# Optimization experiments

Hardware: AMD Instinct MI355X
Metric: run time of the kernel (lower is better)

The kernel has to match this reference:

```python
import jax, jax.numpy as jnp
import numpy as np

N, T, P = 4096, 4096, 12  # series, timesteps, seasonality period


def setup_inputs() -> dict:
    key = jax.random.key(0)
    ks = jax.random.split(key, 8)
    return {
        "alpha": jax.random.uniform(ks[0], (N,), dtype=jnp.float32),
        "beta": jax.random.uniform(ks[1], (N,), dtype=jnp.float32),
        "gamma": jax.random.uniform(ks[2], (N,), dtype=jnp.float32),
        "init_level": jax.random.normal(ks[3], (N,), dtype=jnp.float32),
        "init_trend": jax.random.normal(ks[4], (N,), dtype=jnp.float32) * 0.01,
        "init_seasonal": jax.random.normal(ks[5], (N, P), dtype=jnp.float32),
        "obs_noise": jax.random.normal(ks[6], (N, T), dtype=jnp.float32),
        "err": jax.random.normal(ks[7], (N, T), dtype=jnp.float32),
    }


def reference(alpha, beta, gamma, init_level, init_trend, init_seasonal, obs_noise, err):
    """ETS 'AAA' (additive error/trend/seasonal) recurrence, vectorized over N series.

    Per timestep t (matching the torch loop with model_type='AAA'):
      current = level + trend + seasonal[t % P]
      y[t]    = current + obs_noise[t] * 0.1
      level'  = alpha*(current + err[t]) + (1-alpha)*(level + trend)
      trend'  = beta*(level' - level) + (1-beta)*trend
      seasonal[t % P] = gamma*err[t] + (1-gamma)*seasonal[t % P]
    """
    Tlen = obs_noise.shape[1]
    Pn = init_seasonal.shape[1]

    def step(carry, xs):
        level, trend, seasonal = carry  # (N,), (N,), (N, P)
        t, on, e = xs                   # scalar, (N,), (N,)
        idx = t % Pn
        s_t = seasonal[:, idx]
        current = level + trend + s_t
        y = current + on * 0.1
        new_level = alpha * (current + e) + (1.0 - alpha) * (level + trend)
        new_trend = beta * (new_level - level) + (1.0 - beta) * trend
        new_seasonal = seasonal.at[:, idx].set(gamma * e + (1.0 - gamma) * s_t)
        return (new_level, new_trend, new_seasonal), y

    xs = (jnp.arange(Tlen), obs_noise.T, err.T)  # scan over time
    _, ys = jax.lax.scan(step, (init_level, init_trend, init_seasonal), xs)
    return ys.T  # (N, T)
```

## Files before the change

kernel.cpp:

```cpp
#include <hip/hip_runtime.h>

#define DEV static __device__ __forceinline__

#define SKEW4(j) ((j) + (((j) >> 7) << 2))

DEV float elem(const float4& v, int j) {
  switch (j & 3) {
    case 0: return v.x;
    case 1: return v.y;
    case 2: return v.z;
    default: return v.w;
  }
}
DEV void setelem(float4& v, int j, float x) {
  switch (j & 3) {
    case 0: v.x = x; break;
    case 1: v.y = x; break;
    case 2: v.z = x; break;
    default: v.w = x; break;
  }
}

__global__ __launch_bounds__(128) void ets_w2(
    const float* __restrict__ alpha_, const float* __restrict__ beta_,
    const float* __restrict__ gamma_, const float* __restrict__ lvl0,
    const float* __restrict__ tr0, const float* __restrict__ seas0,
    const float* __restrict__ obs, const float* __restrict__ err,
    float* __restrict__ out, int T)
{
  __shared__ __align__(16) float er_s[4224];
  __shared__ float tot[20];

  const int n = blockIdx.x;
  const int tid = threadIdx.x;
  const int lane = tid & 63;
  const int wv = tid >> 6;

  const float4* ER4 = reinterpret_cast<const float4*>(err + (size_t)n * T);
  const float4* OB4 = reinterpret_cast<const float4*>(obs + (size_t)n * T);
  const int nf4 = T >> 2;

  for (int i = tid; i < nf4; i += 128) {
    float4 e = ER4[i];
    *reinterpret_cast<float4*>(&er_s[SKEW4(i << 2)]) = e;
  }

  float4 O[8];
#pragma unroll
  for (int k = 0; k < 8; ++k) {
    int i = tid + (k << 7);
    if (i < nf4) O[k] = OB4[i];
  }

  const float a = alpha_[n], b = beta_[n], g = gamma_[n];
  const float ab = a * b, ig = 1.0f - g;

  const int nper = T / 12;
  const int base = nper >> 7, rem = nper & 127;
  const int m  = base + (tid < rem ? 1 : 0);
  const int p0 = tid * base + min(tid, rem);
  const int t0 = p0 * 12;

  __syncthreads();

  float l = 0.f, tr = 0.f, s[12];
#pragma unroll
  for (int j = 0; j < 12; ++j) s[j] = 0.f;
  {
    int t = t0;
    for (int u = 0; u < m; ++u, t += 12) {
      float4 e0 = *reinterpret_cast<const float4*>(&er_s[SKEW4(t)]);
      float4 e1 = *reinterpret_cast<const float4*>(&er_s[SKEW4(t + 4)]);
      float4 e2 = *reinterpret_cast<const float4*>(&er_s[SKEW4(t + 8)]);
#pragma unroll
      for (int j = 0; j < 12; ++j) {
        float e = elem(j < 4 ? e0 : (j < 8 ? e1 : e2), j);
        float se = s[j] + e;
        float lt = l + tr;
        l  = fmaf(a, se, lt);
        tr = fmaf(ab, se, tr);
        s[j] = fmaf(g, e, ig * s[j]);
      }
    }
  }

  float S0 = 0.f, S1 = 0.f, dk = 1.f;
  for (int k = 0; k < m; ++k) { S0 += dk; S1 += (float)k * dk; dk *= ig; }
  float GL = 12.0f * (float)m;
  float Gd = dk;
  float Gf = ab * S0;
  float GA = fmaf(a, S0, ab * ((GL - 1.0f) * S0 - 12.0f * S1));
  float Pl = l, Pt = tr, Ps[12];
#pragma unroll
  for (int j = 0; j < 12; ++j) Ps[j] = s[j];

#pragma unroll
  for (int dlt = 1; dlt < 64; dlt <<= 1) {
    float oL  = __shfl_up(GL, dlt, 64);
    float od  = __shfl_up(Gd, dlt, 64);
    float of  = __shfl_up(Gf, dlt, 64);
    float oA  = __shfl_up(GA, dlt, 64);
    float oPl = __shfl_up(Pl, dlt, 64);
    float oPt = __shfl_up(Pt, dlt, 64);
    float oPs[12];
#pragma unroll
    for (int j = 0; j < 12; ++j) oPs[j] = __shfl_up(Ps[j], dlt, 64);
    if (lane >= dlt) {
      float S = 0.f, W = 0.f;
#pragma unroll
      for (int j = 0; j < 12; ++j) {
        S += oPs[j];
        W = fmaf((float)j, oPs[j], W);
      }
      float dot = GA * S - Gf * W;
      float nPl = oPl + GL * oPt + dot + Pl;
      float nPt = fmaf(Gf, S, oPt) + Pt;
#pragma unroll
      for (int j = 0; j < 12; ++j) Ps[j] = fmaf(Gd, oPs[j], Ps[j]);
      GA = oA + GL * of + GA * od;
      Pl = nPl; Pt = nPt;
      Gf = of + Gf * od;
      Gd = od * Gd;
      GL = oL + GL;
    }
  }

  if (wv == 0 && lane == 63) {
    tot[0] = GL; tot[1] = Gd; tot[2] = Gf; tot[3] = GA; tot[4] = Pl; tot[5] = Pt;
#pragma unroll
    for (int j = 0; j < 12; ++j) tot[6 + j] = Ps[j];
  }
  __syncthreads();

  float xl = lvl0[n], xt = tr0[n], xs[12];
#pragma unroll
  for (int j = 0; j < 12; ++j) xs[j] = seas0[(size_t)n * 12 + j];
  if (wv == 1) {
    float ss = 0.f, sw = 0.f;
#pragma unroll
    for (int j = 0; j < 12; ++j) {
      ss += xs[j];
      sw = fmaf((float)j, xs[j], sw);
    }
    float cdot = tot[3] * ss - tot[2] * sw;
    float nxl = xl + tot[0] * xt + cdot + tot[4];
    float nxt = fmaf(tot[2], ss, xt) + tot[5];
#pragma unroll
    for (int j = 0; j < 12; ++j) xs[j] = fmaf(tot[1], xs[j], tot[6 + j]);
    xl = nxl; xt = nxt;
  }

  float ss = 0.f, sw = 0.f;
#pragma unroll
  for (int j = 0; j < 12; ++j) {
    ss += xs[j];
    sw = fmaf((float)j, xs[j], sw);
  }
  float cdot = GA * ss - Gf * sw;
  float yl = xl + GL * xt + cdot + Pl;
  float yt = fmaf(Gf, ss, xt) + Pt;
  float ys[12];
#pragma unroll
  for (int j = 0; j < 12; ++j) ys[j] = fmaf(Gd, xs[j], Ps[j]);

  l  = __shfl_up(yl, 1, 64);
  tr = __shfl_up(yt, 1, 64);
#pragma unroll
  for (int j = 0; j < 12; ++j) s[j] = __shfl_up(ys[j], 1, 64);
  if (lane == 0) {
    l = xl; tr = xt;
#pragma unroll
    for (int j = 0; j < 12; ++j) s[j] = xs[j];
  }

  {
    int t = t0;
    for (int u = 0; u < m; ++u, t += 12) {
      float4* a0 = reinterpret_cast<float4*>(&er_s[SKEW4(t)]);
      float4* a1 = reinterpret_cast<float4*>(&er_s[SKEW4(t + 4)]);
      float4* a2 = reinterpret_cast<float4*>(&er_s[SKEW4(t + 8)]);
      float4 e0 = *a0, e1 = *a1, e2 = *a2;
      float4 y0, y1, y2;
#pragma unroll
      for (int j = 0; j < 12; ++j) {
        float e = elem(j < 4 ? e0 : (j < 8 ? e1 : e2), j);
        float lt = l + tr;
        float cur = lt + s[j];
        float4& yd = (j < 4 ? y0 : (j < 8 ? y1 : y2));
        setelem(yd, j, cur);
        float se = s[j] + e;
        l  = fmaf(a, se, lt);
        tr = fmaf(ab, se, tr);
        s[j] = fmaf(g, e, ig * s[j]);
      }
      *a0 = y0; *a1 = y1; *a2 = y2;
    }
  }
  if (tid == 127) {
    int tt = nper * 12;
    int tail = T - tt;
#pragma unroll
    for (int j = 0; j < 11; ++j) {
      if (j < tail) {
        int ad = SKEW4(tt + j);
        float e = er_s[ad];
        float lt = l + tr;
        float cur = lt + s[j];
        er_s[ad] = cur;
        float se = s[j] + e;
        l  = fmaf(a, se, lt);
        tr = fmaf(ab, se, tr);
        s[j] = fmaf(g, e, ig * s[j]);
      }
    }
  }

  __syncthreads();

  float4* Y4 = reinterpret_cast<float4*>(out + (size_t)n * T);
#pragma unroll
  for (int k = 0; k < 8; ++k) {
    int i = tid + (k << 7);
    if (i < nf4) {
      float4 c = *reinterpret_cast<const float4*>(&er_s[SKEW4(i << 2)]);
      Y4[i] = make_float4(fmaf(O[k].x, 0.1f, c.x), fmaf(O[k].y, 0.1f, c.y),
                          fmaf(O[k].z, 0.1f, c.z), fmaf(O[k].w, 0.1f, c.w));
    }
  }
}

__global__ void ets_gen(
    const float* __restrict__ alpha_, const float* __restrict__ beta_,
    const float* __restrict__ gamma_, const float* __restrict__ lvl0,
    const float* __restrict__ tr0, const float* __restrict__ seas0,
    const float* __restrict__ obs, const float* __restrict__ err,
    float* __restrict__ out, int N, int T, int P)
{
  extern __shared__ float smem[];
  int n = blockIdx.x * blockDim.x + threadIdx.x;
  if (n >= N) return;
  float* s = smem + (size_t)threadIdx.x * P;
  for (int j = 0; j < P; ++j) s[j] = seas0[(size_t)n * P + j];

  float a = alpha_[n], b = beta_[n], g = gamma_[n];
  float ia = 1.0f - a, ib = 1.0f - b, ig = 1.0f - g;
  float level = lvl0[n], trend = tr0[n];

  const float* on = obs + (size_t)n * T;
  const float* er = err + (size_t)n * T;
  float*       yo = out + (size_t)n * T;

  int idx = 0;
  for (int t = 0; t < T; ++t) {
    float onj = on[t], ej = er[t];
    float sj  = s[idx];
    float cur = level + trend + sj;
    yo[t] = fmaf(onj, 0.1f, cur);
    float lt  = level + trend;
    float nl  = fmaf(a, cur + ej, ia * lt);
    float nt  = fmaf(b, nl - level, ib * trend);
    s[idx]    = fmaf(g, ej, ig * sj);
    level = nl; trend = nt;
    if (++idx == P) idx = 0;
  }
}

extern "C" void kernel_launch(void* const* d_in, const int* in_sizes, int n_in,
                              void* d_out, int out_size, void* d_ws, size_t ws_size,
                              hipStream_t stream) {
  (void)n_in; (void)out_size; (void)d_ws; (void)ws_size;
  const float* alpha = (const float*)d_in[0];
  const float* beta  = (const float*)d_in[1];
  const float* gamma = (const float*)d_in[2];
  const float* lvl0  = (const float*)d_in[3];
  const float* tr0   = (const float*)d_in[4];
  const float* seas0 = (const float*)d_in[5];
  const float* obs   = (const float*)d_in[6];
  const float* err   = (const float*)d_in[7];
  float* y = (float*)d_out;

  int N = in_sizes[0];
  int P = in_sizes[5] / N;
  int T = in_sizes[6] / N;

  if (P == 12 && (T % 4) == 0 && T >= 12 && T <= 4096) {
    ets_w2<<<dim3(N), dim3(128), 0, stream>>>(
        alpha, beta, gamma, lvl0, tr0, seas0, obs, err, y, T);
  } else {
    int bs = 64;
    size_t sh = (size_t)bs * (size_t)P * sizeof(float);
    ets_gen<<<dim3((N + bs - 1) / bs), dim3(bs), sh, stream>>>(
        alpha, beta, gamma, lvl0, tr0, seas0, obs, err, y, N, T, P);
  }
}
```

Before: 44.86 us.

## Keep err chunks in registers and write outputs directly from second pass

Each thread now keeps its err values in a fixed array of up to three periods of registers, so the second pass no longer re-reads them from shared memory. The obs prefetch and the final shared-memory staging pass are removed: each thread reads obs and writes y directly to global memory in 48-byte float4 chunks, which also drops the last __syncthreads. The trade-off is less coalesced global access, since each thread's chunks are contiguous but strided across lanes. The register caching assumes at most three periods per thread (T<=4096 with 128 threads); for larger m the code would silently skip work, though the launcher limits T to 4096.

```diff
diff --git a/kernel.cpp b/kernel.cpp
--- a/kernel.cpp
+++ b/kernel.cpp
@@ -21,7 +21,7 @@
   }
 }
 
-__global__ __launch_bounds__(128) void ets_w2(
+__global__ __launch_bounds__(128) void ets_w2r(
     const float* __restrict__ alpha_, const float* __restrict__ beta_,
     const float* __restrict__ gamma_, const float* __restrict__ lvl0,
     const float* __restrict__ tr0, const float* __restrict__ seas0,
@@ -37,19 +37,11 @@
   const int wv = tid >> 6;
 
   const float4* ER4 = reinterpret_cast<const float4*>(err + (size_t)n * T);
-  const float4* OB4 = reinterpret_cast<const float4*>(obs + (size_t)n * T);
   const int nf4 = T >> 2;
 
   for (int i = tid; i < nf4; i += 128) {
     float4 e = ER4[i];
     *reinterpret_cast<float4*>(&er_s[SKEW4(i << 2)]) = e;
-  }
-
-  float4 O[8];
-#pragma unroll
-  for (int k = 0; k < 8; ++k) {
-    int i = tid + (k << 7);
-    if (i < nf4) O[k] = OB4[i];
   }
 
   const float a = alpha_[n], b = beta_[n], g = gamma_[n];
@@ -63,23 +55,27 @@
 
   __syncthreads();
 
+  float4 E[9];
   float l = 0.f, tr = 0.f, s[12];
 #pragma unroll
   for (int j = 0; j < 12; ++j) s[j] = 0.f;
   {
     int t = t0;
-    for (int u = 0; u < m; ++u, t += 12) {
-      float4 e0 = *reinterpret_cast<const float4*>(&er_s[SKEW4(t)]);
-      float4 e1 = *reinterpret_cast<const float4*>(&er_s[SKEW4(t + 4)]);
-      float4 e2 = *reinterpret_cast<const float4*>(&er_s[SKEW4(t + 8)]);
-#pragma unroll
-      for (int j = 0; j < 12; ++j) {
-        float e = elem(j < 4 ? e0 : (j < 8 ? e1 : e2), j);
-        float se = s[j] + e;
-        float lt = l + tr;
-        l  = fmaf(a, se, lt);
-        tr = fmaf(ab, se, tr);
-        s[j] = fmaf(g, e, ig * s[j]);
+#pragma unroll
+    for (int u = 0; u < 3; ++u, t += 12) {
+      if (u < m) {
+        E[u * 3 + 0] = *reinterpret_cast<const float4*>(&er_s[SKEW4(t)]);
+        E[u * 3 + 1] = *reinterpret_cast<const float4*>(&er_s[SKEW4(t + 4)]);
+        E[u * 3 + 2] = *reinterpret_cast<const float4*>(&er_s[SKEW4(t + 8)]);
+#pragma unroll
+        for (int j = 0; j < 12; ++j) {
+          float e = elem(E[u * 3 + (j >> 2)], j);
+          float se = s[j] + e;
+          float lt = l + tr;
+          l  = fmaf(a, se, lt);
+          tr = fmaf(ab, se, tr);
+          s[j] = fmaf(g, e, ig * s[j]);
+        }
       }
     }
   }
@@ -173,58 +169,51 @@
     for (int j = 0; j < 12; ++j) s[j] = xs[j];
   }
 
-  {
-    int t = t0;
-    for (int u = 0; u < m; ++u, t += 12) {
-      float4* a0 = reinterpret_cast<float4*>(&er_s[SKEW4(t)]);
-      float4* a1 = reinterpret_cast<float4*>(&er_s[SKEW4(t + 4)]);
-      float4* a2 = reinterpret_cast<float4*>(&er_s[SKEW4(t + 8)]);
-      float4 e0 = *a0, e1 = *a1, e2 = *a2;
+  const float* ob = obs + (size_t)n * T + (size_t)p0 * 12;
+  float*       yo = out + (size_t)n * T + (size_t)p0 * 12;
+#pragma unroll
+  for (int u = 0; u < 3; ++u) {
+    if (u < m) {
+      const float4* o4 = reinterpret_cast<const float4*>(ob + u * 12);
+      float4 O0 = o4[0], O1 = o4[1], O2 = o4[2];
       float4 y0, y1, y2;
 #pragma unroll
       for (int j = 0; j < 12; ++j) {
-        float e = elem(j < 4 ? e0 : (j < 8 ? e1 : e2), j);
+        float e  = elem(E[u * 3 + (j >> 2)], j);
+        float oj = elem(j < 4 ? O0 : (j < 8 ? O1 : O2), j);
         float lt = l + tr;
         float cur = lt + s[j];
         float4& yd = (j < 4 ? y0 : (j < 8 ? y1 : y2));
-        setelem(yd, j, cur);
+        setelem(yd, j, fmaf(oj, 0.1f, cur));
         float se = s[j] + e;
         l  = fmaf(a, se, lt);
         tr = fmaf(ab, se, tr);
         s[j] = fmaf(g, e, ig * s[j]);
       }
-      *a0 = y0; *a1 = y1; *a2 = y2;
-    }
-  }
+      float4* y4 = reinterpret_cast<float4*>(yo + u * 12);
+      y4[0] = y0; y4[1] = y1; y4[2] = y2;
+    }
+  }
+
   if (tid == 127) {
     int tt = nper * 12;
     int tail = T - tt;
-#pragma unroll
-    for (int j = 0; j < 11; ++j) {
-      if (j < tail) {
-        int ad = SKEW4(tt + j);
-        float e = er_s[ad];
-        float lt = l + tr;
-        float cur = lt + s[j];
-        er_s[ad] = cur;
-        float se = s[j] + e;
-        l  = fmaf(a, se, lt);
-        tr = fmaf(ab, se, tr);
-        s[j] = fmaf(g, e, ig * s[j]);
-      }
-    }
-  }
-
-  __syncthreads();
-
-  float4* Y4 = reinterpret_cast<float4*>(out + (size_t)n * T);
-#pragma unroll
-  for (int k = 0; k < 8; ++k) {
-    int i = tid + (k << 7);
-    if (i < nf4) {
-      float4 c = *reinterpret_cast<const float4*>(&er_s[SKEW4(i << 2)]);
-      Y4[i] = make_float4(fmaf(O[k].x, 0.1f, c.x), fmaf(O[k].y, 0.1f, c.y),
-                          fmaf(O[k].z, 0.1f, c.z), fmaf(O[k].w, 0.1f, c.w));
+    if (tail > 0) {
+      const float* ot = obs + (size_t)n * T + tt;
+      float*       yt2 = out + (size_t)n * T + tt;
+#pragma unroll
+      for (int j = 0; j < 11; ++j) {
+        if (j < tail) {
+          float e = er_s[SKEW4(tt + j)];
+          float lt = l + tr;
+          float cur = lt + s[j];
+          yt2[j] = fmaf(ot[j], 0.1f, cur);
+          float se = s[j] + e;
+          l  = fmaf(a, se, lt);
+          tr = fmaf(ab, se, tr);
+          s[j] = fmaf(g, e, ig * s[j]);
+        }
+      }
     }
   }
 }
@@ -284,7 +273,7 @@
   int T = in_sizes[6] / N;
 
   if (P == 12 && (T % 4) == 0 && T >= 12 && T <= 4096) {
-    ets_w2<<<dim3(N), dim3(128), 0, stream>>>(
+    ets_w2r<<<dim3(N), dim3(128), 0, stream>>>(
         alpha, beta, gamma, lvl0, tr0, seas0, obs, err, y, T);
   } else {
     int bs = 64;
```

After: 53.70 us. +19.7%, slower.
